# Performance work log

Hardware: AMD Instinct MI355X
Metric: run time of the kernel (lower is better)

## Reference

```python
import jax, jax.numpy as jnp
import numpy as np


def setup_inputs() -> dict:
    key = jax.random.key(0)
    ks = jax.random.split(key, 11)
    B, Cin, H, W = 4, 3, 256, 256
    width, m1, m2, L = 64, 16, 16, 4
    def n(k, shape, scale=1.0):
        return (scale * jax.random.normal(k, shape)).astype(jnp.float32)
    spec_scale = 1.0 / (width * width)  # matches torch scale = 1/(in_ch*out_ch)
    return {
        "x": n(ks[0], (B, Cin, H, W)),
        "fc0_w": n(ks[1], (width, Cin), 0.1),
        "fc0_b": n(ks[2], (width,), 0.1),
        "spec_wr": n(ks[3], (L, width, width, m1, m2), spec_scale),
        "spec_wi": n(ks[4], (L, width, width, m1, m2), spec_scale),
        "w_w": n(ks[5], (L, width, width), 0.1),
        "w_b": n(ks[6], (L, width), 0.1),
        "fc1_w": n(ks[7], (128, width), 0.1),
        "fc1_b": n(ks[8], (128,), 0.1),
        "fc2_w": n(ks[9], (1, 128), 0.1),
        "fc2_b": n(ks[10], (1,), 0.1),
    }


def conv1x1(x, w, b):
    # x: (B,C,H,W), w: (O,C), b: (O,) -- equivalent to nn.Conv2d(C,O,1)
    return jnp.einsum('bchw,oc->bohw', x, w) + b[None, :, None, None]


def spectral_conv2d(x, wr, wi):
    # x: (B,C,H,W); wr/wi: (C,O,m1,m2) real/imag parts of cfloat weight
    B, C, H, W = x.shape
    m1, m2 = wr.shape[2], wr.shape[3]
    O = wr.shape[1]
    x_ft = jnp.fft.rfft2(x)                       # (B,C,H,W//2+1) complex64
    w = wr + 1j * wi
    blk = jnp.einsum('bixy,ioxy->boxy', x_ft[:, :, :m1, :m2], w)
    out_ft = jnp.zeros((B, O, H, W // 2 + 1), dtype=blk.dtype)
    out_ft = out_ft.at[:, :, :m1, :m2].set(blk)
    return jnp.fft.irfft2(out_ft, s=(H, W))


def reference(x, fc0_w, fc0_b, spec_wr, spec_wi, w_w, w_b, fc1_w, fc1_b, fc2_w, fc2_b):
    h = conv1x1(x, fc0_w, fc0_b)
    n_layers = spec_wr.shape[0]
    for i in range(n_layers):
        h = spectral_conv2d(h, spec_wr[i], spec_wi[i]) + conv1x1(h, w_w[i], w_b[i])
        h = jax.nn.gelu(h, approximate=False)
    h = jax.nn.gelu(conv1x1(h, fc1_w, fc1_b), approximate=False)
    return conv1x1(h, fc2_w, fc2_b)
```

## Files before the change

### kernel.cpp

```cpp
#include <hip/hip_runtime.h>
#include <math.h>

#define HW 65536

typedef __attribute__((ext_vector_type(8))) short short8;
typedef __attribute__((ext_vector_type(4))) float f32x4;

__device__ __forceinline__ unsigned bf16rne(float f) {
  union { float f; unsigned u; } a; a.f = f;
  return (a.u + 0x7fffu + ((a.u >> 16) & 1u)) >> 16;
}
__device__ __forceinline__ float bf16tof(unsigned h) {
  union { unsigned u; float f; } a; a.u = h << 16;
  return a.f;
}
__device__ __forceinline__ float gelu(float v) {
  float ax = fabsf(v) * 0.70710678118654752f;
  float t = 1.0f / fmaf(0.3275911f, ax, 1.0f);
  float p = t * (0.254829592f +
           t * (-0.284496736f +
           t * (1.421413741f +
           t * (-1.453152027f +
           t * 1.061405429f))));
  float e = __expf(-ax * ax);
  float er = copysignf(fmaf(-p, e, 1.0f), v);
  return 0.5f * v * (1.0f + er);
}

__global__ __launch_bounds__(256) void k_tables(float* __restrict__ cosT, float* __restrict__ sinT,
                                                ushort* __restrict__ eah, ushort* __restrict__ eal,
                                                ushort* __restrict__ e2h, ushort* __restrict__ e2l,
                                                const float* __restrict__ ww, const float* __restrict__ w1,
                                                ushort* __restrict__ wh, ushort* __restrict__ wl,
                                                ushort* __restrict__ w1h, ushort* __restrict__ w1l) {
  int idx = blockIdx.x * 256 + threadIdx.x;
  const float w = 0.0245436926061702596f;
  if (idx < 4096) {
    int k = idx >> 8, xx = idx & 255;
    int t = (k * xx) & 255;
    float ang = (float)t * w;
    cosT[idx] = cosf(ang);
    sinT[idx] = sinf(ang);
  } else if (idx < 12288) {
    int e = idx - 4096;
    int j = e >> 8, xx = e & 255;
    int k = j >> 1;
    int t = (k * xx) & 255;
    float ang = (float)t * w;
    float val = (j & 1) ? -sinf(ang) : cosf(ang);
    unsigned hi = bf16rne(val);
    unsigned lo = bf16rne(val - bf16tof(hi));
    eah[j * 256 + xx] = (ushort)hi;
    eal[j * 256 + xx] = (ushort)lo;
    e2h[xx * 32 + j] = (ushort)hi;
    e2l[xx * 32 + j] = (ushort)lo;
  } else if (idx < 28672) {
    int j = idx - 12288;
    float v = ww[j];
    unsigned hi = bf16rne(v);
    wh[j] = (ushort)hi;
    wl[j] = (ushort)bf16rne(v - bf16tof(hi));
  } else {
    int j = idx - 28672;
    float v = w1[j];
    unsigned hi = bf16rne(v);
    w1h[j] = (ushort)hi;
    w1l[j] = (ushort)bf16rne(v - bf16tof(hi));
  }
}

__global__ __launch_bounds__(256) void k_fc0(const float* __restrict__ x, const float* __restrict__ w,
                                             const float* __restrict__ b,
                                             const ushort* __restrict__ eah, const ushort* __restrict__ eal,
                                             ushort* __restrict__ hh, float* __restrict__ A) {
  int bid = blockIdx.x;
  int bb = bid >> 8, y = bid & 255;
  int tid = threadIdx.x;
  __shared__ float ws[192];
  __shared__ float bs[64];
  __shared__ __align__(16) ushort XsH[256 * 66];
  if (tid < 192) ws[tid] = w[tid];
  if (tid < 64) bs[tid] = b[tid];
  __syncthreads();
  const float* xrow = x + ((size_t)(bb * 3) * 256 + y) * 256;
#pragma unroll
  for (int rep = 0; rep < 8; ++rep) {
    int flat = rep * 256 + tid;
    int p = flat >> 3, q = flat & 7;
    float v0 = xrow[p], v1 = xrow[p + HW], v2 = xrow[p + 2 * HW];
    short8 H;
#pragma unroll
    for (int i = 0; i < 8; ++i) {
      int o = q * 8 + i;
      float v = bs[o] + ws[o * 3] * v0 + ws[o * 3 + 1] * v1 + ws[o * 3 + 2] * v2;
      H[i] = (short)bf16rne(v);
    }
    size_t nb = ((size_t)bid * 256 + p) * 64 + q * 8;
    *(short8*)&hh[nb] = H;
    *(short8*)&XsH[p * 66 + q * 8] = H;
  }
  __syncthreads();
  int lane = tid & 63, wv = tid >> 6;
  int lm = lane & 15, lg = lane >> 4;
  f32x4 d0 = (f32x4){0.f, 0.f, 0.f, 0.f};
  f32x4 d1 = (f32x4){0.f, 0.f, 0.f, 0.f};
  int c = wv * 16 + lm;
#pragma unroll
  for (int kc = 0; kc < 8; ++kc) {
    int x0 = kc * 32 + lg * 8;
    short8 bh;
#pragma unroll
    for (int i = 0; i < 8; ++i) bh[i] = (short)XsH[(x0 + i) * 66 + c];
    short8 a0h = *(const short8*)&eah[lm * 256 + x0];
    short8 a0l = *(const short8*)&eal[lm * 256 + x0];
    short8 a1h = *(const short8*)&eah[(16 + lm) * 256 + x0];
    short8 a1l = *(const short8*)&eal[(16 + lm) * 256 + x0];
    d0 = __builtin_amdgcn_mfma_f32_16x16x32_bf16(a0h, bh, d0, 0, 0, 0);
    d0 = __builtin_amdgcn_mfma_f32_16x16x32_bf16(a0l, bh, d0, 0, 0, 0);
    d1 = __builtin_amdgcn_mfma_f32_16x16x32_bf16(a1h, bh, d1, 0, 0, 0);
    d1 = __builtin_amdgcn_mfma_f32_16x16x32_bf16(a1l, bh, d1, 0, 0, 0);
  }
  size_t row = ((size_t)(bb * 64 + c) * 256 + y) * 32;
  *(float4*)&A[row + lg * 4] = make_float4(d0[0], d0[1], d0[2], d0[3]);
  *(float4*)&A[row + 16 + lg * 4] = make_float4(d1[0], d1[1], d1[2], d1[3]);
}

__global__ __launch_bounds__(256) void k_f2(const float* __restrict__ A, const float* __restrict__ cosT,
                                            const float* __restrict__ sinT, float2* __restrict__ Xp) {
  int bid = blockIdx.x;
  int plane = bid >> 1, yh = bid & 1;
  int tid = threadIdx.x;
  __shared__ float2 As[128 * 16];
  __shared__ float ct[16 * 129];
  __shared__ float stt[16 * 129];
  const float2* Ap = (const float2*)A + (size_t)plane * 4096;
#pragma unroll
  for (int rep = 0; rep < 8; ++rep) {
    int flat = rep * 256 + tid;
    As[flat] = Ap[yh * 2048 + flat];
  }
#pragma unroll
  for (int rep = 0; rep < 8; ++rep) {
    int flat = rep * 256 + tid;
    int ky = flat >> 7, yp = flat & 127;
    ct[ky * 129 + yp] = cosT[ky * 256 + yh * 128 + yp];
    stt[ky * 129 + yp] = sinT[ky * 256 + yh * 128 + yp];
  }
  __syncthreads();
  int ky = tid >> 4, kx = tid & 15;
  float xr = 0.f, xi = 0.f;
#pragma unroll 4
  for (int yp = 0; yp < 128; ++yp) {
    float2 a = As[yp * 16 + kx];
    float c = ct[ky * 129 + yp], s = stt[ky * 129 + yp];
    xr += c * a.x + s * a.y;
    xi += c * a.y - s * a.x;
  }
  Xp[(size_t)plane * 512 + yh * 256 + tid] = make_float2(xr, xi);
}

__global__ __launch_bounds__(256) void k_mix(const float2* __restrict__ Xp, const float* __restrict__ wr,
                                             const float* __restrict__ wi, float2* __restrict__ Y) {
  int o = blockIdx.x >> 2;
  int mc = blockIdx.x & 3;
  int tid = threadIdx.x;
  int cg = tid >> 6, m2 = tid & 63;
  int m = mc * 64 + m2;
  float yr[4] = {0.f, 0.f, 0.f, 0.f}, yi[4] = {0.f, 0.f, 0.f, 0.f};
#pragma unroll 4
  for (int cc = 0; cc < 16; ++cc) {
    int c = cg * 16 + cc;
    float r = wr[(c * 64 + o) * 256 + m];
    float im = wi[(c * 64 + o) * 256 + m];
#pragma unroll
    for (int b = 0; b < 4; ++b) {
      size_t pb = (size_t)(b * 64 + c) * 512;
      float2 x0 = Xp[pb + m];
      float2 x1 = Xp[pb + 256 + m];
      float xvx = x0.x + x1.x, xvy = x0.y + x1.y;
      yr[b] += xvx * r - xvy * im;
      yi[b] += xvx * im + xvy * r;
    }
  }
  __shared__ float2 red[1024];
#pragma unroll
  for (int b = 0; b < 4; ++b) red[cg * 256 + b * 64 + m2] = make_float2(yr[b], yi[b]);
  __syncthreads();
  int b = tid >> 6;
  float sx = 0.f, sy = 0.f;
#pragma unroll
  for (int g2 = 0; g2 < 4; ++g2) {
    float2 v = red[g2 * 256 + b * 64 + m2];
    sx += v.x; sy += v.y;
  }
  Y[(b * 64 + o) * 256 + m] = make_float2(sx, sy);
}

__global__ __launch_bounds__(256) void k_inv1(const float2* __restrict__ Y, const float* __restrict__ cosT,
                                              const float* __restrict__ sinT,
                                              ushort* __restrict__ gh, ushort* __restrict__ gl) {
  int plane = blockIdx.x;
  int y = threadIdx.x;
  __shared__ float2 Ys[256];
  Ys[threadIdx.x] = Y[plane * 256 + threadIdx.x];
  __syncthreads();
  float gr[16], gi[16];
#pragma unroll
  for (int k = 0; k < 16; ++k) { gr[k] = 0.f; gi[k] = 0.f; }
  for (int ky = 0; ky < 16; ++ky) {
    float c = cosT[ky * 256 + y], s = sinT[ky * 256 + y];
#pragma unroll
    for (int kx = 0; kx < 16; ++kx) {
      float2 v = Ys[ky * 16 + kx];
      gr[kx] += c * v.x - s * v.y;
      gi[kx] += c * v.y + s * v.x;
    }
  }
  float val[32];
  const float sc = 1.0f / 65536.0f;
#pragma unroll
  for (int kx = 0; kx < 16; ++kx) {
    float m = (kx == 0) ? sc : 2.0f * sc;
    val[2 * kx] = gr[kx] * m;
    val[2 * kx + 1] = gi[kx] * m;
  }
  size_t gb = ((size_t)plane * 256 + y) * 32;
#pragma unroll
  for (int q = 0; q < 8; ++q) {
    ushort4 H, L;
#pragma unroll
    for (int r = 0; r < 4; ++r) {
      float v = val[q * 4 + r];
      unsigned hi = bf16rne(v);
      ((ushort*)&H)[r] = (ushort)hi;
      ((ushort*)&L)[r] = (ushort)bf16rne(v - bf16tof(hi));
    }
    *(ushort4*)&gh[gb + q * 4] = H;
    *(ushort4*)&gl[gb + q * 4] = L;
  }
}

__global__ __launch_bounds__(256) void k_layer(const ushort* __restrict__ hh,
                                               const ushort* __restrict__ gh, const ushort* __restrict__ gl,
                                               const ushort* __restrict__ wh, const ushort* __restrict__ wl,
                                               const float* __restrict__ wb,
                                               const ushort* __restrict__ e2h, const ushort* __restrict__ e2l,
                                               const ushort* __restrict__ eah, const ushort* __restrict__ eal,
                                               ushort* __restrict__ oh,
                                               float* __restrict__ A, int do_dft) {
  int bid = blockIdx.x;
  int b = bid >> 8, y = bid & 255;
  int tid = threadIdx.x;
  int lane = tid & 63, wv = tid >> 6;
  int lm = lane & 15, lg = lane >> 4;
  size_t nbase = (size_t)(b * 256 + y) * 256;

  __shared__ __align__(16) ushort smem[16896];
  __shared__ float wbs[64];
  ushort* wsH = smem;
  ushort* wsL = smem + 4608;
  ushort* gsH = smem + 9216;
  ushort* gsL = smem + 11776;
  ushort* Xs  = smem;

#pragma unroll
  for (int rep = 0; rep < 2; ++rep) {
    int flat = rep * 2048 + tid * 8;
    int o = flat >> 6, cc = flat & 63;
    *(short8*)&wsH[o * 72 + cc] = *(const short8*)&wh[flat];
    *(short8*)&wsL[o * 72 + cc] = *(const short8*)&wl[flat];
  }
  {
    int o = tid >> 2, i = (tid & 3) * 8;
    size_t ga = ((size_t)(b * 64 + o) * 256 + y) * 32 + i;
    *(short8*)&gsH[o * 40 + i] = *(const short8*)&gh[ga];
    *(short8*)&gsL[o * 40 + i] = *(const short8*)&gl[ga];
  }
  if (tid < 64) wbs[tid] = wb[tid];
  __syncthreads();

  short8 bh0[4], bh1[4], ehv[4], elv[4];
#pragma unroll
  for (int ni = 0; ni < 4; ++ni) {
    int xx = wv * 64 + ni * 16 + lm;
    size_t hb = (nbase + xx) * 64 + lg * 8;
    bh0[ni] = *(const short8*)&hh[hb];
    bh1[ni] = *(const short8*)&hh[hb + 32];
    ehv[ni] = *(const short8*)&e2h[xx * 32 + lg * 8];
    elv[ni] = *(const short8*)&e2l[xx * 32 + lg * 8];
  }

  f32x4 acc[4][4];
#pragma unroll
  for (int mi = 0; mi < 4; ++mi)
#pragma unroll
    for (int ni = 0; ni < 4; ++ni) acc[mi][ni] = (f32x4){0.f, 0.f, 0.f, 0.f};

#pragma unroll
  for (int mi = 0; mi < 4; ++mi) {
    int o = mi * 16 + lm;
    short8 ah0 = *(const short8*)&wsH[o * 72 + lg * 8];
    short8 al0 = *(const short8*)&wsL[o * 72 + lg * 8];
    short8 ah1 = *(const short8*)&wsH[o * 72 + 32 + lg * 8];
    short8 al1 = *(const short8*)&wsL[o * 72 + 32 + lg * 8];
    short8 gah = *(const short8*)&gsH[o * 40 + lg * 8];
    short8 gal = *(const short8*)&gsL[o * 40 + lg * 8];
#pragma unroll
    for (int ni = 0; ni < 4; ++ni) {
      acc[mi][ni] = __builtin_amdgcn_mfma_f32_16x16x32_bf16(ah0, bh0[ni], acc[mi][ni], 0, 0, 0);
      acc[mi][ni] = __builtin_amdgcn_mfma_f32_16x16x32_bf16(al0, bh0[ni], acc[mi][ni], 0, 0, 0);
      acc[mi][ni] = __builtin_amdgcn_mfma_f32_16x16x32_bf16(ah1, bh1[ni], acc[mi][ni], 0, 0, 0);
      acc[mi][ni] = __builtin_amdgcn_mfma_f32_16x16x32_bf16(al1, bh1[ni], acc[mi][ni], 0, 0, 0);
      acc[mi][ni] = __builtin_amdgcn_mfma_f32_16x16x32_bf16(gah, ehv[ni], acc[mi][ni], 0, 0, 0);
      acc[mi][ni] = __builtin_amdgcn_mfma_f32_16x16x32_bf16(gah, elv[ni], acc[mi][ni], 0, 0, 0);
      acc[mi][ni] = __builtin_amdgcn_mfma_f32_16x16x32_bf16(gal, ehv[ni], acc[mi][ni], 0, 0, 0);
    }
  }

  __syncthreads();
#pragma unroll
  for (int mi = 0; mi < 4; ++mi)
#pragma unroll
    for (int ni = 0; ni < 4; ++ni) {
      int xx = wv * 64 + ni * 16 + lm;
      ushort4 H;
#pragma unroll
      for (int r = 0; r < 4; ++r) {
        int o = mi * 16 + lg * 4 + r;
        float ge = gelu(acc[mi][ni][r] + wbs[o]);
        ((ushort*)&H)[r] = (ushort)bf16rne(ge);
      }
      *(ushort4*)&Xs[xx * 66 + mi * 16 + lg * 4] = H;
    }
  __syncthreads();
#pragma unroll
  for (int rep = 0; rep < 8; ++rep) {
    int flat = rep * 256 + tid;
    int p = flat >> 3, off = (flat & 7) * 8;
    short8 vH = *(const short8*)&Xs[p * 66 + off];
    *(short8*)&oh[(nbase + p) * 64 + off] = vH;
  }

  if (do_dft) {
    f32x4 d0 = (f32x4){0.f, 0.f, 0.f, 0.f};
    f32x4 d1 = (f32x4){0.f, 0.f, 0.f, 0.f};
    int c = wv * 16 + lm;
#pragma unroll
    for (int kc = 0; kc < 8; ++kc) {
      int x0 = kc * 32 + lg * 8;
      short8 bh;
#pragma unroll
      for (int i = 0; i < 8; ++i) bh[i] = (short)Xs[(x0 + i) * 66 + c];
      short8 a0h = *(const short8*)&eah[lm * 256 + x0];
      short8 a0l = *(const short8*)&eal[lm * 256 + x0];
      short8 a1h = *(const short8*)&eah[(16 + lm) * 256 + x0];
      short8 a1l = *(const short8*)&eal[(16 + lm) * 256 + x0];
      d0 = __builtin_amdgcn_mfma_f32_16x16x32_bf16(a0h, bh, d0, 0, 0, 0);
      d0 = __builtin_amdgcn_mfma_f32_16x16x32_bf16(a0l, bh, d0, 0, 0, 0);
      d1 = __builtin_amdgcn_mfma_f32_16x16x32_bf16(a1h, bh, d1, 0, 0, 0);
      d1 = __builtin_amdgcn_mfma_f32_16x16x32_bf16(a1l, bh, d1, 0, 0, 0);
    }
    size_t row = ((size_t)(b * 64 + c) * 256 + y) * 32;
    *(float4*)&A[row + lg * 4] = make_float4(d0[0], d0[1], d0[2], d0[3]);
    *(float4*)&A[row + 16 + lg * 4] = make_float4(d1[0], d1[1], d1[2], d1[3]);
  }
}

__global__ __launch_bounds__(256) void k_final(const ushort* __restrict__ hh,
                                               const ushort* __restrict__ w1h, const ushort* __restrict__ w1l,
                                               const float* __restrict__ b1, const float* __restrict__ w2,
                                               const float* __restrict__ b2, float* __restrict__ out) {
  int bid = blockIdx.x;
  int b = bid >> 10, y = (bid >> 2) & 255, xq = bid & 3;
  int tid = threadIdx.x;
  int lane = tid & 63, wave = tid >> 6;
  int lm = lane & 15, lg = lane >> 4;
  int x = xq * 64 + wave * 16 + lm;
  size_t nb = (size_t)(b * 256 + y) * 256 + x;

  __shared__ __align__(16) ushort w1sH[128 * 72], w1sL[128 * 72];
  __shared__ float b1s[128], w2s[128];

#pragma unroll
  for (int rep = 0; rep < 4; ++rep) {
    int flat = rep * 2048 + tid * 8;
    int j = flat >> 6, cc = flat & 63;
    *(short8*)&w1sH[j * 72 + cc] = *(const short8*)&w1h[flat];
    *(short8*)&w1sL[j * 72 + cc] = *(const short8*)&w1l[flat];
  }
  if (tid < 128) { b1s[tid] = b1[tid]; w2s[tid] = w2[tid]; }
  __syncthreads();

  short8 bh0 = *(const short8*)&hh[nb * 64 + lg * 8];
  short8 bh1 = *(const short8*)&hh[nb * 64 + 32 + lg * 8];

  f32x4 acc[8];
#pragma unroll
  for (int mi = 0; mi < 8; ++mi) acc[mi] = (f32x4){0.f, 0.f, 0.f, 0.f};

#pragma unroll
  for (int mi = 0; mi < 8; ++mi) {
    int j = mi * 16 + lm;
    short8 ah0 = *(const short8*)&w1sH[j * 72 + lg * 8];
    short8 al0 = *(const short8*)&w1sL[j * 72 + lg * 8];
    acc[mi] = __builtin_amdgcn_mfma_f32_16x16x32_bf16(ah0, bh0, acc[mi], 0, 0, 0);
    acc[mi] = __builtin_amdgcn_mfma_f32_16x16x32_bf16(al0, bh0, acc[mi], 0, 0, 0);
    short8 ah1 = *(const short8*)&w1sH[j * 72 + 32 + lg * 8];
    short8 al1 = *(const short8*)&w1sL[j * 72 + 32 + lg * 8];
    acc[mi] = __builtin_amdgcn_mfma_f32_16x16x32_bf16(ah1, bh1, acc[mi], 0, 0, 0);
    acc[mi] = __builtin_amdgcn_mfma_f32_16x16x32_bf16(al1, bh1, acc[mi], 0, 0, 0);
  }

  float p = 0.f;
#pragma unroll
  for (int mi = 0; mi < 8; ++mi)
#pragma unroll
    for (int r = 0; r < 4; ++r) {
      int j = mi * 16 + lg * 4 + r;
      p += w2s[j] * gelu(acc[mi][r] + b1s[j]);
    }
  p += __shfl_xor(p, 16);
  p += __shfl_xor(p, 32);
  if (lg == 0) {
    out[(b * 256 + y) * 256 + x] = p + b2[0];
  }
}

extern "C" void kernel_launch(void* const* d_in, const int* in_sizes, int n_in,
                              void* d_out, int out_size, void* d_ws, size_t ws_size,
                              hipStream_t stream) {
  const float* x       = (const float*)d_in[0];
  const float* fc0_w   = (const float*)d_in[1];
  const float* fc0_b   = (const float*)d_in[2];
  const float* spec_wr = (const float*)d_in[3];
  const float* spec_wi = (const float*)d_in[4];
  const float* w_w     = (const float*)d_in[5];
  const float* w_b     = (const float*)d_in[6];
  const float* fc1_w   = (const float*)d_in[7];
  const float* fc1_b   = (const float*)d_in[8];
  const float* fc2_w   = (const float*)d_in[9];
  const float* fc2_b   = (const float*)d_in[10];
  float* out = (float*)d_out;

  char* ws = (char*)d_ws;
  ushort* h0h  = (ushort*)ws;
  ushort* h1h  = (ushort*)(ws + 33554432);
  float*  A    = (float*)(ws + 67108864);
  ushort* gh   = (ushort*)(ws + 75497472);
  ushort* gl   = (ushort*)(ws + 79691776);
  float2* Xp   = (float2*)(ws + 83886080);
  float2* Y    = (float2*)(ws + 84934656);
  float*  cosT = (float*)(ws + 85458944);
  float*  sinT = (float*)(ws + 85475328);
  ushort* eah  = (ushort*)(ws + 85491712);
  ushort* eal  = (ushort*)(ws + 85508096);
  ushort* e2h  = (ushort*)(ws + 85524480);
  ushort* e2l  = (ushort*)(ws + 85540864);
  ushort* wWh  = (ushort*)(ws + 85557248);
  ushort* wWl  = (ushort*)(ws + 85590016);
  ushort* w1h  = (ushort*)(ws + 85622784);
  ushort* w1l  = (ushort*)(ws + 85639168);

  k_tables<<<144, 256, 0, stream>>>(cosT, sinT, eah, eal, e2h, e2l,
                                    w_w, fc1_w, wWh, wWl, w1h, w1l);
  k_fc0<<<1024, 256, 0, stream>>>(x, fc0_w, fc0_b, eah, eal, h0h, A);
  ushort* hch = h0h;
  ushort* hnh = h1h;
  for (int l = 0; l < 4; ++l) {
    k_f2<<<512, 256, 0, stream>>>(A, cosT, sinT, Xp);
    k_mix<<<256, 256, 0, stream>>>(Xp, spec_wr + (size_t)l * 1048576, spec_wi + (size_t)l * 1048576, Y);
    k_inv1<<<256, 256, 0, stream>>>(Y, cosT, sinT, gh, gl);
    k_layer<<<1024, 256, 0, stream>>>(hch, gh, gl, wWh + l * 4096, wWl + l * 4096,
                                      w_b + l * 64, e2h, e2l, eah, eal, hnh, A, (l < 3) ? 1 : 0);
    ushort* t = hch; hch = hnh; hnh = t;
  }
  k_final<<<4096, 256, 0, stream>>>(hch, w1h, w1l, fc1_b, fc2_w, fc2_b, out);
}
```

Before: 342.3 us.

## Fuse spectral mode mixing with first inverse DFT stage per (o,b) block

Merges the spectral weight-mixing kernel and the first inverse-DFT kernel into one, with each block now computing all 256 modes for one output channel and batch. The mixed spectrum stays in shared memory instead of being written to and re-read from a global Y buffer, and one launch per layer is removed. In exchange, spectral weights are no longer reused across batches within a block, so weight reads from memory or cache grow fourfold.

```diff
diff --git a/kernel.cpp b/kernel.cpp
--- a/kernel.cpp
+++ b/kernel.cpp
@@ -159,51 +159,50 @@
   Xp[(size_t)plane * 512 + yh * 256 + tid] = make_float2(xr, xi);
 }
 
-__global__ __launch_bounds__(256) void k_mix(const float2* __restrict__ Xp, const float* __restrict__ wr,
-                                             const float* __restrict__ wi, float2* __restrict__ Y) {
-  int o = blockIdx.x >> 2;
-  int mc = blockIdx.x & 3;
+__global__ __launch_bounds__(256) void k_mixinv(const float2* __restrict__ Xp,
+                                                const float* __restrict__ wr, const float* __restrict__ wi,
+                                                const float* __restrict__ cosT, const float* __restrict__ sinT,
+                                                ushort* __restrict__ gh, ushort* __restrict__ gl) {
+  int bid = blockIdx.x;
+  int o = bid >> 2, b = bid & 3;
   int tid = threadIdx.x;
   int cg = tid >> 6, m2 = tid & 63;
-  int m = mc * 64 + m2;
+  __shared__ float2 red[1024];
+  __shared__ float2 Ys[256];
+
   float yr[4] = {0.f, 0.f, 0.f, 0.f}, yi[4] = {0.f, 0.f, 0.f, 0.f};
 #pragma unroll 4
   for (int cc = 0; cc < 16; ++cc) {
     int c = cg * 16 + cc;
-    float r = wr[(c * 64 + o) * 256 + m];
-    float im = wi[(c * 64 + o) * 256 + m];
-#pragma unroll
-    for (int b = 0; b < 4; ++b) {
-      size_t pb = (size_t)(b * 64 + c) * 512;
+    size_t wbx = (size_t)(c * 64 + o) * 256;
+    size_t pb = (size_t)(b * 64 + c) * 512;
+#pragma unroll
+    for (int mc = 0; mc < 4; ++mc) {
+      int m = mc * 64 + m2;
+      float r = wr[wbx + m];
+      float im = wi[wbx + m];
       float2 x0 = Xp[pb + m];
       float2 x1 = Xp[pb + 256 + m];
       float xvx = x0.x + x1.x, xvy = x0.y + x1.y;
-      yr[b] += xvx * r - xvy * im;
-      yi[b] += xvx * im + xvy * r;
-    }
-  }
-  __shared__ float2 red[1024];
-#pragma unroll
-  for (int b = 0; b < 4; ++b) red[cg * 256 + b * 64 + m2] = make_float2(yr[b], yi[b]);
-  __syncthreads();
-  int b = tid >> 6;
-  float sx = 0.f, sy = 0.f;
-#pragma unroll
-  for (int g2 = 0; g2 < 4; ++g2) {
-    float2 v = red[g2 * 256 + b * 64 + m2];
-    sx += v.x; sy += v.y;
-  }
-  Y[(b * 64 + o) * 256 + m] = make_float2(sx, sy);
-}
-
-__global__ __launch_bounds__(256) void k_inv1(const float2* __restrict__ Y, const float* __restrict__ cosT,
-                                              const float* __restrict__ sinT,
-                                              ushort* __restrict__ gh, ushort* __restrict__ gl) {
-  int plane = blockIdx.x;
-  int y = threadIdx.x;
-  __shared__ float2 Ys[256];
-  Ys[threadIdx.x] = Y[plane * 256 + threadIdx.x];
-  __syncthreads();
+      yr[mc] += xvx * r - xvy * im;
+      yi[mc] += xvx * im + xvy * r;
+    }
+  }
+#pragma unroll
+  for (int mc = 0; mc < 4; ++mc) red[cg * 256 + mc * 64 + m2] = make_float2(yr[mc], yi[mc]);
+  __syncthreads();
+  {
+    float sx = 0.f, sy = 0.f;
+#pragma unroll
+    for (int g2 = 0; g2 < 4; ++g2) {
+      float2 v = red[g2 * 256 + tid];
+      sx += v.x; sy += v.y;
+    }
+    Ys[tid] = make_float2(sx, sy);
+  }
+  __syncthreads();
+
+  int y = tid;
   float gr[16], gi[16];
 #pragma unroll
   for (int k = 0; k < 16; ++k) { gr[k] = 0.f; gi[k] = 0.f; }
@@ -224,7 +223,7 @@
     val[2 * kx] = gr[kx] * m;
     val[2 * kx + 1] = gi[kx] * m;
   }
-  size_t gb = ((size_t)plane * 256 + y) * 32;
+  size_t gb = ((size_t)(b * 64 + o) * 256 + y) * 32;
 #pragma unroll
   for (int q = 0; q < 8; ++q) {
     ushort4 H, L;
@@ -449,7 +448,6 @@
   ushort* gh   = (ushort*)(ws + 75497472);
   ushort* gl   = (ushort*)(ws + 79691776);
   float2* Xp   = (float2*)(ws + 83886080);
-  float2* Y    = (float2*)(ws + 84934656);
   float*  cosT = (float*)(ws + 85458944);
   float*  sinT = (float*)(ws + 85475328);
   ushort* eah  = (ushort*)(ws + 85491712);
@@ -468,8 +466,8 @@
   ushort* hnh = h1h;
   for (int l = 0; l < 4; ++l) {
     k_f2<<<512, 256, 0, stream>>>(A, cosT, sinT, Xp);
-    k_mix<<<256, 256, 0, stream>>>(Xp, spec_wr + (size_t)l * 1048576, spec_wi + (size_t)l * 1048576, Y);
-    k_inv1<<<256, 256, 0, stream>>>(Y, cosT, sinT, gh, gl);
+    k_mixinv<<<256, 256, 0, stream>>>(Xp, spec_wr + (size_t)l * 1048576,
+                                      spec_wi + (size_t)l * 1048576, cosT, sinT, gh, gl);
     k_layer<<<1024, 256, 0, stream>>>(hch, gh, gl, wWh + l * 4096, wWl + l * 4096,
                                       w_b + l * 64, e2h, e2l, eah, eal, hnh, A, (l < 3) ? 1 : 0);
     ushort* t = hch; hch = hnh; hnh = t;
```

New measurement: 344.6 us. About the same (+0.7%).
